# Kernel optimization log

Hardware: AMD Instinct MI355X
Metric: run time of the kernel (lower is better)

Reference implementation:

```python
import jax, jax.numpy as jnp
import numpy as np

B, T, E, V, H = 2, 2048, 1024, 2048, 8
KD, HD = E // H, V // H  # key_dim=128, head_dim=256
EPS = 1e-6


def rotate_every_two(x):
    x1 = x[..., ::2]
    x2 = x[..., 1::2]
    return jnp.stack((-x2, x1), axis=-1).reshape(x.shape)


def theta_shift(x, sin, cos):
    return x * cos + rotate_every_two(x) * sin


def setup_inputs() -> dict:
    key = jax.random.key(0)
    ks = jax.random.split(key, 8)
    x = jax.random.normal(ks[0], (B, T, E), dtype=jnp.float32)
    angle = jnp.arange(T, dtype=jnp.float32)[:, None] * (1.0 / (10000.0 ** (jnp.repeat(jnp.arange(KD // 2, dtype=jnp.float32), 2) * 2.0 / KD)))
    sin = jnp.sin(angle)  # [T, KD]
    cos = jnp.cos(angle)
    # RetNet per-head causal decay mask: decay_h = 1 - 2^(-5-h)
    decay = 1.0 - 2.0 ** (-5.0 - jnp.arange(H, dtype=jnp.float32))  # [H]
    idx = jnp.arange(T, dtype=jnp.float32)
    diff = idx[:, None] - idx[None, :]  # n - m
    causal = diff >= 0
    mask = jnp.where(causal[None], jnp.exp(jnp.where(causal, diff, 0.0)[None] * jnp.log(decay)[:, None, None]), 0.0)  # [H,T,T]
    g = 2 ** (-2.5)
    Wq = jax.random.normal(ks[1], (E, E), dtype=jnp.float32) * (g * np.sqrt(2.0 / (E + E)))
    Wk = jax.random.normal(ks[2], (E, E), dtype=jnp.float32) * (g * np.sqrt(2.0 / (E + E)))
    Wv = jax.random.normal(ks[3], (E, V), dtype=jnp.float32) * (g * np.sqrt(2.0 / (E + V)))
    Wg = jax.random.normal(ks[4], (E, V), dtype=jnp.float32) * (g * np.sqrt(2.0 / (E + V)))
    Wo = jax.random.normal(ks[5], (V, E), dtype=jnp.float32) * np.sqrt(2.0 / (V + E))
    return {"x": x, "sin": sin, "cos": cos, "mask": mask,
            "Wq": Wq, "Wk": Wk, "Wv": Wv, "Wg": Wg, "Wo": Wo}


def reference(x, sin, cos, mask, Wq, Wk, Wv, Wg, Wo):
    b, t, _ = x.shape
    scaling = KD ** -0.5
    q = (x @ Wq).reshape(b, t, H, KD).transpose(0, 2, 1, 3)  # [B,H,T,KD]
    k = (x @ Wk * scaling).reshape(b, t, H, KD).transpose(0, 2, 1, 3)
    v = x @ Wv  # [B,T,V]
    g = x @ Wg
    qr = theta_shift(q, sin, cos)
    kr = theta_shift(k, sin, cos)
    vr = v.reshape(b, t, H, HD).transpose(0, 2, 1, 3)  # [B,H,T,HD]
    qk = jnp.einsum('bhsk,bhtk->bhst', qr, kr) * mask  # [B,H,T,T]
    denom = jnp.clip(jnp.abs(jax.lax.stop_gradient(qk).sum(-1, keepdims=True)), 1.0, None)
    qk = qk / denom
    out = jnp.einsum('bhst,bhtd->bhsd', qk, vr)  # [B,H,T,HD]
    out = out.transpose(0, 2, 1, 3)  # [B,T,H,HD]
    # RMSNorm over head_dim, no affine
    out = out * jax.lax.rsqrt(jnp.mean(out * out, axis=-1, keepdims=True) + EPS)
    out = out.reshape(b, t, H * HD)
    out = jax.nn.silu(g) * out
    return out @ Wo  # [B,T,E]
```

## Files before the change

### kernel.cpp

```cpp
#include <hip/hip_runtime.h>
#include <hip/hip_bf16.h>


#define B_ 2
#define T_ 2048
#define E_ 1024
#define V_ 2048
#define H_ 8
#define KD_ 128
#define HD_ 256
#define M_ 4096

typedef __attribute__((ext_vector_type(8))) short bf16x8;
typedef __attribute__((ext_vector_type(4))) float f32x4;

__device__ __forceinline__ float u2f(unsigned short u) {
    return __uint_as_float(((unsigned)u) << 16);
}
__device__ __forceinline__ unsigned short f2bu(float f) {
    unsigned x = __float_as_uint(f);
    return (unsigned short)((x + 0x7fffu + ((x >> 16) & 1u)) >> 16);
}

typedef const __attribute__((address_space(1))) void gas_t;
typedef __attribute__((address_space(3))) void las_t;
__device__ __forceinline__ void gl_lds16(const void* g, void* l) {
    __builtin_amdgcn_global_load_lds((gas_t*)g, (las_t*)l, 16, 0, 0);
}

__global__ __launch_bounds__(256) void conv_x_kernel(
    const float* __restrict__ x, unsigned short* __restrict__ xb)
{
    const size_t i = ((size_t)blockIdx.x * 256 + threadIdx.x) * 8;
    float4 a = *(const float4*)(x + i);
    float4 c = *(const float4*)(x + i + 4);
    *(ushort4*)(xb + i)     = make_ushort4(f2bu(a.x), f2bu(a.y), f2bu(a.z), f2bu(a.w));
    *(ushort4*)(xb + i + 4) = make_ushort4(f2bu(c.x), f2bu(c.y), f2bu(c.z), f2bu(c.w));
}

__global__ __launch_bounds__(256) void transW4_kernel(
    const float* __restrict__ Wq, const float* __restrict__ Wk,
    const float* __restrict__ Wv, const float* __restrict__ Wg,
    unsigned short* __restrict__ Wt)
{
    const int z = blockIdx.z;
    const float* W; int N; int rofs;
    if (z == 0)      { W = Wq; N = 1024; rofs = 0; }
    else if (z == 1) { W = Wk; N = 1024; rofs = 1024; }
    else if (z == 2) { W = Wv; N = 2048; rofs = 2048; }
    else             { W = Wg; N = 2048; rofs = 4096; }
    const int n0 = blockIdx.x * 64;
    if (n0 >= N) return;
    const int k0 = blockIdx.y * 64;

    __shared__ float tl[64][65];
    const int tid = threadIdx.x;
    #pragma unroll
    for (int i = 0; i < 4; ++i) {
        int kr = i * 16 + (tid >> 4);
        int nc = (tid & 15) * 4;
        float4 v = *(const float4*)(W + (size_t)(k0 + kr) * N + n0 + nc);
        tl[kr][nc] = v.x; tl[kr][nc + 1] = v.y; tl[kr][nc + 2] = v.z; tl[kr][nc + 3] = v.w;
    }
    __syncthreads();
    #pragma unroll
    for (int i = 0; i < 4; ++i) {
        int nr = i * 16 + (tid >> 4);
        int kc = (tid & 15) * 4;
        ushort4 u = make_ushort4(f2bu(tl[kc + 0][nr]), f2bu(tl[kc + 1][nr]),
                                 f2bu(tl[kc + 2][nr]), f2bu(tl[kc + 3][nr]));
        *(ushort4*)(Wt + (size_t)(rofs + n0 + nr) * E_ + k0 + kc) = u;
    }
}

__global__ __launch_bounds__(256) void transW_kernel(
    const float* __restrict__ W, unsigned short* __restrict__ Wt, int K, int N)
{
    __shared__ float tl[64][65];
    const int tid = threadIdx.x;
    const int n0 = blockIdx.x * 64, k0 = blockIdx.y * 64;
    #pragma unroll
    for (int i = 0; i < 4; ++i) {
        int kr = i * 16 + (tid >> 4);
        int nc = (tid & 15) * 4;
        float4 v = *(const float4*)(W + (size_t)(k0 + kr) * N + n0 + nc);
        tl[kr][nc] = v.x; tl[kr][nc + 1] = v.y; tl[kr][nc + 2] = v.z; tl[kr][nc + 3] = v.w;
    }
    __syncthreads();
    #pragma unroll
    for (int i = 0; i < 4; ++i) {
        int nr = i * 16 + (tid >> 4);
        int kc = (tid & 15) * 4;
        ushort4 u = make_ushort4(f2bu(tl[kc + 0][nr]), f2bu(tl[kc + 1][nr]),
                                 f2bu(tl[kc + 2][nr]), f2bu(tl[kc + 3][nr]));
        *(ushort4*)(Wt + (size_t)(n0 + nr) * K + k0 + kc) = u;
    }
}

__global__ __launch_bounds__(256) void transV_kernel(
    const unsigned short* __restrict__ vb, unsigned short* __restrict__ vt)
{
    __shared__ unsigned short tl[64][68];
    const int tid = threadIdx.x;
    const int t0 = blockIdx.x * 64, c0 = blockIdx.y * 64, b = blockIdx.z;
    #pragma unroll
    for (int i = 0; i < 4; ++i) {
        int tr = i * 16 + (tid >> 4);
        int cc = (tid & 15) * 4;
        ushort4 v = *(const ushort4*)(vb + (size_t)(b * T_ + t0 + tr) * V_ + c0 + cc);
        tl[tr][cc] = v.x; tl[tr][cc + 1] = v.y; tl[tr][cc + 2] = v.z; tl[tr][cc + 3] = v.w;
    }
    __syncthreads();
    #pragma unroll
    for (int i = 0; i < 4; ++i) {
        int cr = i * 16 + (tid >> 4);
        int tc = (tid & 15) * 4;
        ushort4 u = make_ushort4(tl[tc + 0][cr], tl[tc + 1][cr], tl[tc + 2][cr], tl[tc + 3][cr]);
        *(ushort4*)(vt + (size_t)(b * V_ + c0 + cr) * T_ + t0 + tc) = u;
    }
}

#define GSTAGE(BUF, K0)                                                        \
    {                                                                          \
        _Pragma("unroll")                                                      \
        for (int i = 0; i < 4; ++i) {                                          \
            int r = i * 32 + srow;                                             \
            int cb = scolb ^ ((r & 7) << 4);                                   \
            gl_lds16((const char*)(A  + (size_t)(rowBase + r) * K + (K0)) + cb,\
                     Asm[BUF] + i * 4096 + w * 1024);                          \
            gl_lds16((const char*)(Bt + (size_t)(colBase + r) * K + (K0)) + cb,\
                     Bsm[BUF] + i * 4096 + w * 1024);                          \
        }                                                                      \
    }

#define GCOMPUTE(BUF)                                                          \
    {                                                                          \
        _Pragma("unroll")                                                      \
        for (int kk = 0; kk < 2; ++kk) {                                       \
            const int cb = kk * 64 + (l >> 4) * 16;                            \
            bf16x8 a[4], b[4];                                                 \
            _Pragma("unroll")                                                  \
            for (int m = 0; m < 4; ++m) {                                      \
                int r = wr * 64 + m * 16 + (l & 15);                           \
                a[m] = *(const bf16x8*)(Asm[BUF] + r * 128 + (cb ^ ((r & 7) << 4))); \
            }                                                                  \
            _Pragma("unroll")                                                  \
            for (int n = 0; n < 4; ++n) {                                      \
                int r = wc * 64 + n * 16 + (l & 15);                           \
                b[n] = *(const bf16x8*)(Bsm[BUF] + r * 128 + (cb ^ ((r & 7) << 4))); \
            }                                                                  \
            _Pragma("unroll")                                                  \
            for (int m = 0; m < 4; ++m)                                        \
                _Pragma("unroll")                                              \
                for (int n = 0; n < 4; ++n)                                    \
                    acc[m][n] = __builtin_amdgcn_mfma_f32_16x16x32_bf16(a[m], b[n], acc[m][n], 0, 0, 0); \
        }                                                                      \
    }

#define GEMM_PIPELINE_LOOP                                                     \
    GSTAGE(0, 0)                                                               \
    const int nk = K / 64;                                                     \
    for (int kt = 0; kt < nk; ++kt) {                                          \
        const int cur = kt & 1;                                                \
        if (kt + 1 < nk) {                                                     \
            GSTAGE(1 - cur, (kt + 1) * 64)                                     \
            asm volatile("s_waitcnt vmcnt(8)" ::: "memory");                   \
        } else {                                                               \
            asm volatile("s_waitcnt vmcnt(0)" ::: "memory");                   \
        }                                                                      \
        __builtin_amdgcn_s_barrier();                                          \
        __builtin_amdgcn_sched_barrier(0);                                     \
        GCOMPUTE(cur)                                                          \
        __builtin_amdgcn_s_barrier();                                          \
        __builtin_amdgcn_sched_barrier(0);                                     \
    }

__global__ __launch_bounds__(256) void gemm_qkvg_kernel(
    const unsigned short* __restrict__ A,
    const unsigned short* __restrict__ Bt,
    unsigned short* __restrict__ qb,
    unsigned short* __restrict__ kb,
    unsigned short* __restrict__ vb,
    unsigned short* __restrict__ gb)
{
    const int K = E_;
    __shared__ __align__(16) char Asm[2][128 * 64 * 2];
    __shared__ __align__(16) char Bsm[2][128 * 64 * 2];
    const int tid = threadIdx.x;
    const int l = tid & 63;
    const int w = tid >> 6;
    const int wr = w >> 1, wc = w & 1;
    const int rowBase = blockIdx.y * 128;
    const int colBase = blockIdx.x * 128;
    const int srow = tid >> 3;
    const int scolb = (tid & 7) * 16;

    f32x4 acc[4][4] = {};

    GEMM_PIPELINE_LOOP

    const int colW = colBase + wc * 64;
    unsigned short* dst;
    int cofs, stride;
    if (colW < 1024)      { dst = qb; cofs = 0;    stride = E_; }
    else if (colW < 2048) { dst = kb; cofs = 1024; stride = E_; }
    else if (colW < 4096) { dst = vb; cofs = 2048; stride = V_; }
    else                  { dst = gb; cofs = 4096; stride = V_; }
    #pragma unroll
    for (int m = 0; m < 4; ++m)
        #pragma unroll
        for (int n = 0; n < 4; ++n)
            #pragma unroll
            for (int r = 0; r < 4; ++r) {
                int row = rowBase + wr * 64 + m * 16 + (l >> 4) * 4 + r;
                int col = colW + n * 16 + (l & 15);
                float f = acc[m][n][r];
                if (!isfinite(f)) f = 0.f;
                dst[(size_t)row * stride + (col - cofs)] = f2bu(f);
            }
}

__global__ __launch_bounds__(256) void gemm_wo_kernel(
    const unsigned short* __restrict__ A,
    const unsigned short* __restrict__ Bt,
    float* __restrict__ C)
{
    const int K = V_;
    __shared__ __align__(16) char Asm[2][64 * 128];
    __shared__ __align__(16) char Bsm[2][128 * 128];
    const int tid = threadIdx.x;
    const int l = tid & 63;
    const int w = tid >> 6;
    const int wr = w >> 1, wc = w & 1;
    const int rowBase = blockIdx.y * 64;
    const int colBase = blockIdx.x * 128;
    const int srow = tid >> 3;
    const int scolb = (tid & 7) * 16;

    f32x4 acc[2][4] = {};

#define WSTAGE(BUF, K0)                                                        \
    {                                                                          \
        _Pragma("unroll")                                                      \
        for (int i = 0; i < 2; ++i) {                                          \
            int r = i * 32 + srow;                                             \
            int cb = scolb ^ ((r & 7) << 4);                                   \
            gl_lds16((const char*)(A + (size_t)(rowBase + r) * K + (K0)) + cb, \
                     Asm[BUF] + i * 4096 + w * 1024);                          \
        }                                                                      \
        _Pragma("unroll")                                                      \
        for (int i = 0; i < 4; ++i) {                                          \
            int r = i * 32 + srow;                                             \
            int cb = scolb ^ ((r & 7) << 4);                                   \
            gl_lds16((const char*)(Bt + (size_t)(colBase + r) * K + (K0)) + cb,\
                     Bsm[BUF] + i * 4096 + w * 1024);                          \
        }                                                                      \
    }

    WSTAGE(0, 0)
    const int nk = K / 64;
    for (int kt = 0; kt < nk; ++kt) {
        const int cur = kt & 1;
        if (kt + 1 < nk) {
            WSTAGE(1 - cur, (kt + 1) * 64)
            asm volatile("s_waitcnt vmcnt(6)" ::: "memory");
        } else {
            asm volatile("s_waitcnt vmcnt(0)" ::: "memory");
        }
        __builtin_amdgcn_s_barrier();
        __builtin_amdgcn_sched_barrier(0);
        #pragma unroll
        for (int kk = 0; kk < 2; ++kk) {
            const int cb = kk * 64 + (l >> 4) * 16;
            bf16x8 a[2], b[4];
            #pragma unroll
            for (int m = 0; m < 2; ++m) {
                int r = wr * 32 + m * 16 + (l & 15);
                a[m] = *(const bf16x8*)(Asm[cur] + r * 128 + (cb ^ ((r & 7) << 4)));
            }
            #pragma unroll
            for (int n = 0; n < 4; ++n) {
                int r = wc * 64 + n * 16 + (l & 15);
                b[n] = *(const bf16x8*)(Bsm[cur] + r * 128 + (cb ^ ((r & 7) << 4)));
            }
            #pragma unroll
            for (int m = 0; m < 2; ++m)
                #pragma unroll
                for (int n = 0; n < 4; ++n)
                    acc[m][n] = __builtin_amdgcn_mfma_f32_16x16x32_bf16(a[m], b[n], acc[m][n], 0, 0, 0);
        }
        __builtin_amdgcn_s_barrier();
        __builtin_amdgcn_sched_barrier(0);
    }
#undef WSTAGE

    #pragma unroll
    for (int m = 0; m < 2; ++m)
        #pragma unroll
        for (int n = 0; n < 4; ++n)
            #pragma unroll
            for (int r = 0; r < 4; ++r) {
                int row = rowBase + wr * 32 + m * 16 + (l >> 4) * 4 + r;
                int col = colBase + wc * 64 + n * 16 + (l & 15);
                float f = acc[m][n][r];
                if (!isfinite(f)) f = 0.f;
                C[(size_t)row * E_ + col] = f;
            }
}

__global__ __launch_bounds__(256) void theta2_kernel(
    unsigned short* __restrict__ qb,
    unsigned short* __restrict__ kb,
    const float* __restrict__ sinp, const float* __restrict__ cosp)
{
    unsigned short* qk = blockIdx.y ? kb : qb;
    const float scale = blockIdx.y ? 0.088388347648318447f : 1.0f;
    const int i = blockIdx.x * 256 + threadIdx.x;
    const int pe = i & (E_ / 2 - 1);
    const int bt = i >> 9;
    const int t = bt & (T_ - 1);
    const int e0 = pe << 1;
    const int d0 = e0 & (KD_ - 1);
    const size_t base = (size_t)bt * E_ + e0;
    const float q0 = u2f(qk[base]);
    const float q1 = u2f(qk[base + 1]);
    const int sb = t * KD_ + d0;
    const float s0 = sinp[sb], s1 = sinp[sb + 1];
    const float c0 = cosp[sb], c1 = cosp[sb + 1];
    qk[base]     = f2bu((q0 * c0 - q1 * s0) * scale);
    qk[base + 1] = f2bu((q1 * c1 + q0 * s1) * scale);
}

#define STAGE_K(BUF, T0)                                                       \
    {                                                                          \
        _Pragma("unroll")                                                      \
        for (int i = 0; i < 4; ++i) {                                          \
            int r = i * 16 + (tid >> 4);                                       \
            int cb = ((tid & 15) * 16) ^ ((r & 7) << 4);                       \
            gl_lds16((const char*)(kb + (size_t)(b * T_ + (T0) + r) * E_ + h * KD_) + cb, \
                     Ks[BUF] + i * 4096 + w * 1024);                           \
        }                                                                      \
    }

#define STAGE_V(T0)                                                            \
    {                                                                          \
        _Pragma("unroll")                                                      \
        for (int i = 0; i < 8; ++i) {                                          \
            int r = i * 32 + (tid >> 3);                                       \
            int cb = ((tid & 7) * 16) ^ ((r & 7) << 4);                        \
            gl_lds16((const char*)(vt + (size_t)((b * H_ + h) * HD_ + r) * T_ + (T0)) + cb, \
                     Vs + i * 4096 + w * 1024);                                \
        }                                                                      \
    }

__global__ __launch_bounds__(256, 2) void retention_mfma_kernel(
    const unsigned short* __restrict__ qb,
    const unsigned short* __restrict__ kb,
    const unsigned short* __restrict__ vt,
    const unsigned short* __restrict__ g,
    unsigned short* __restrict__ ao)
{
    __shared__ __align__(16) char Ks[2][64 * 128 * 2];
    __shared__ __align__(16) char Vs[256 * 64 * 2];
    __shared__ __align__(16) char Pq[64 * 64 * 2];
    __shared__ float rsum_p[4][64];
    __shared__ float rsq_p[4][64];
    const int tid = threadIdx.x;
    const int l = tid & 63;
    const int w = tid >> 6;
    const int g_ = l >> 4;
    const int q15 = l & 15;
    const int orig = (int)blockIdx.x;
    const int xcd  = orig & 7;
    const int pos  = orig >> 3;
    const int slot = pos >> 5;
    const int cu   = pos & 31;
    const int half = cu >> 4;
    const int c15  = cu & 15;
    const int bh   = xcd * 2 + half;
    const int chunk = slot ? c15 : (31 - c15);
    const int b = bh >> 3, h = bh & 7;
    const int s0 = chunk * 64;
    const float ld = logf(1.f - exp2f(-5.f - (float)h));

    float es[4];
    #pragma unroll
    for (int qb2 = 0; qb2 < 4; ++qb2)
        es[qb2] = __expf((float)(s0 + qb2 * 16 + q15) * ld);
    float etl[4];
    #pragma unroll
    for (int r = 0; r < 4; ++r)
        etl[r] = __expf(-(float)(w * 16 + 4 * g_ + r) * ld);
    const float Dm64 = __expf(-64.f * ld);
    float etb = 1.f;

    bf16x8 qf[4][4];
    #pragma unroll
    for (int qb2 = 0; qb2 < 4; ++qb2) {
        const char* qp = (const char*)(qb + (size_t)(b * T_ + s0 + qb2 * 16 + q15) * E_ + h * KD_);
        #pragma unroll
        for (int kk = 0; kk < 4; ++kk)
            qf[qb2][kk] = *(const bf16x8*)(qp + kk * 64 + g_ * 16);
    }

    f32x4 oaccT[4][4] = {};
    float rs[4] = {0.f, 0.f, 0.f, 0.f};

    const int nt = chunk + 1;
    STAGE_K(0, 0)

    for (int t = 0; t < nt; ++t) {
        const int cur = t & 1;
        const int t0 = t * 64;
        STAGE_V(t0)
        if (t + 1 < nt) {
            STAGE_K(1 - cur, t0 + 64)
            asm volatile("s_waitcnt vmcnt(12)" ::: "memory");
        } else {
            asm volatile("s_waitcnt vmcnt(8)" ::: "memory");
        }
        __builtin_amdgcn_s_barrier();
        __builtin_amdgcn_sched_barrier(0);

        f32x4 sacc[4] = {};
        {
            const int krow = w * 16 + q15;
            const int swz = (krow & 7) << 4;
            #pragma unroll
            for (int kk = 0; kk < 4; ++kk) {
                bf16x8 kf = *(const bf16x8*)(Ks[cur] + krow * 256 + ((kk * 64 + g_ * 16) ^ swz));
                #pragma unroll
                for (int qb2 = 0; qb2 < 4; ++qb2)
                    sacc[qb2] = __builtin_amdgcn_mfma_f32_16x16x32_bf16(kf, qf[qb2][kk], sacc[qb2], 0, 0, 0);
            }
        }
        {
            const float etw = etb;
            #pragma unroll
            for (int qb2 = 0; qb2 < 4; ++qb2) {
                const int qg = s0 + qb2 * 16 + q15;
                const int q_local = qb2 * 16 + q15;
                float rsp = 0.f;
                unsigned short pk[4];
                #pragma unroll
                for (int r = 0; r < 4; ++r) {
                    int tg = t0 + w * 16 + 4 * g_ + r;
                    float pm = (qg >= tg) ? sacc[qb2][r] * (es[qb2] * etw * etl[r]) : 0.f;
                    rsp += pm;
                    pk[r] = f2bu(pm);
                }
                *(ushort4*)(Pq + q_local * 128 + (((w * 16 + 4 * g_) * 2) ^ ((q_local & 7) << 4))) =
                    make_ushort4(pk[0], pk[1], pk[2], pk[3]);
                rsp += __shfl_xor(rsp, 16);
                rsp += __shfl_xor(rsp, 32);
                rs[qb2] += rsp;
            }
            etb *= Dm64;
        }
        if (t + 1 < nt) {
            asm volatile("s_waitcnt vmcnt(4) lgkmcnt(0)" ::: "memory");
        } else {
            asm volatile("s_waitcnt vmcnt(0) lgkmcnt(0)" ::: "memory");
        }
        __builtin_amdgcn_s_barrier();
        __builtin_amdgcn_sched_barrier(0);
        #pragma unroll
        for (int kk = 0; kk < 2; ++kk) {
            const int cb = kk * 64 + g_ * 16;
            bf16x8 pf[4], vf[4];
            #pragma unroll
            for (int qb2 = 0; qb2 < 4; ++qb2) {
                int pr = qb2 * 16 + q15;
                pf[qb2] = *(const bf16x8*)(Pq + pr * 128 + (cb ^ ((pr & 7) << 4)));
            }
            #pragma unroll
            for (int m = 0; m < 4; ++m) {
                int vr = w * 64 + m * 16 + q15;
                vf[m] = *(const bf16x8*)(Vs + vr * 128 + (cb ^ ((vr & 7) << 4)));
            }
            #pragma unroll
            for (int qb2 = 0; qb2 < 4; ++qb2)
                #pragma unroll
                for (int m = 0; m < 4; ++m)
                    oaccT[qb2][m] = __builtin_amdgcn_mfma_f32_16x16x32_bf16(vf[m], pf[qb2], oaccT[qb2][m], 0, 0, 0);
        }
        __builtin_amdgcn_s_barrier();
        __builtin_amdgcn_sched_barrier(0);
    }

    if (l < 16) {
        #pragma unroll
        for (int qb2 = 0; qb2 < 4; ++qb2)
            rsum_p[w][qb2 * 16 + q15] = rs[qb2];
    }
    __syncthreads();

    float inv[4];
    #pragma unroll
    for (int qb2 = 0; qb2 < 4; ++qb2) {
        const int q_local = qb2 * 16 + q15;
        const float tot = rsum_p[0][q_local] + rsum_p[1][q_local] +
                          rsum_p[2][q_local] + rsum_p[3][q_local];
        inv[qb2] = 1.f / fmaxf(fabsf(tot), 1.f);
    }

    #pragma unroll
    for (int qb2 = 0; qb2 < 4; ++qb2) {
        float ps = 0.f;
        #pragma unroll
        for (int m = 0; m < 4; ++m)
            #pragma unroll
            for (int r = 0; r < 4; ++r) {
                float o = oaccT[qb2][m][r] * inv[qb2];
                ps += o * o;
            }
        ps += __shfl_xor(ps, 16);
        ps += __shfl_xor(ps, 32);
        if (l < 16) rsq_p[w][qb2 * 16 + q15] = ps;
    }
    __syncthreads();

    #pragma unroll
    for (int qb2 = 0; qb2 < 4; ++qb2) {
        const int q_local = qb2 * 16 + q15;
        const float tot = rsq_p[0][q_local] + rsq_p[1][q_local] +
                          rsq_p[2][q_local] + rsq_p[3][q_local];
        const float scale = rsqrtf(tot * (1.0f / HD_) + 1e-6f) * inv[qb2];
        const size_t rowb = (size_t)(b * T_ + s0 + q_local) * V_ + h * HD_;
        #pragma unroll
        for (int m = 0; m < 4; ++m) {
            const int vc0 = w * 64 + m * 16 + 4 * g_;
            ushort4 gv4 = *(const ushort4*)(g + rowb + vc0);
            const unsigned short* gv = (const unsigned short*)&gv4;
            unsigned short outp[4];
            #pragma unroll
            for (int r = 0; r < 4; ++r) {
                const float gvf = u2f(gv[r]);
                const float silu = gvf / (1.f + __expf(-gvf));
                float f = oaccT[qb2][m][r] * scale * silu;
                if (!isfinite(f)) f = 0.f;
                outp[r] = f2bu(f);
            }
            *(ushort4*)(ao + rowb + vc0) = make_ushort4(outp[0], outp[1], outp[2], outp[3]);
        }
    }
}

extern "C" void kernel_launch(void* const* d_in, const int* in_sizes, int n_in,
                              void* d_out, int out_size, void* d_ws, size_t ws_size,
                              hipStream_t stream)
{
    const float* x    = (const float*)d_in[0];
    const float* sinp = (const float*)d_in[1];
    const float* cosp = (const float*)d_in[2];
    const float* Wq   = (const float*)d_in[4];
    const float* Wk   = (const float*)d_in[5];
    const float* Wv   = (const float*)d_in[6];
    const float* Wg   = (const float*)d_in[7];
    const float* Wo   = (const float*)d_in[8];
    float* out = (float*)d_out;

    unsigned short* xb = (unsigned short*)d_out;
    unsigned short* qb = xb + (size_t)M_ * E_;

    char* ws = (char*)d_ws;
    unsigned short* kb  = (unsigned short*)(ws + 0);
    unsigned short* vb  = (unsigned short*)(ws + 8388608);
    unsigned short* gb  = (unsigned short*)(ws + 25165824);
    unsigned short* wt  = (unsigned short*)(ws + 41943040);
    unsigned short* vt  = (unsigned short*)(ws + 54525952);
    unsigned short* aob = (unsigned short*)(ws + 71303168);
    unsigned short* wot = (unsigned short*)(ws + 88080384);

    dim3 blk(256);
    conv_x_kernel<<<M_ * E_ / 8 / 256, blk, 0, stream>>>(x, xb);

    transW4_kernel<<<dim3(32, 16, 4), blk, 0, stream>>>(Wq, Wk, Wv, Wg, wt);

    gemm_qkvg_kernel<<<dim3(48, 32), blk, 0, stream>>>(xb, wt, qb, kb, vb, gb);

    theta2_kernel<<<dim3(M_ * E_ / 2 / 256, 2), blk, 0, stream>>>(qb, kb, sinp, cosp);

    transV_kernel<<<dim3(32, 32, B_), blk, 0, stream>>>(vb, vt);

    retention_mfma_kernel<<<dim3(512), blk, 0, stream>>>(qb, kb, vt, gb, aob);

    transW_kernel<<<dim3(16, 32), blk, 0, stream>>>(Wo, wot, V_, E_);
    gemm_wo_kernel<<<dim3(8, 64), blk, 0, stream>>>(aob, wot, out);
}
```

Baseline: 190.6 us.

## Double-buffer V tiles in retention kernel and fold Wo transpose into weight prep

The retention kernel now keeps two V buffers, so the next V tile is prefetched together with the next K tile instead of being loaded at the top of each iteration and waited on mid-loop. The launch bound's min-blocks hint is dropped and the XCD-aware block-to-chunk mapping is replaced by a simple linear one, heaviest chunks first. The Wo transpose is merged into the combined weight-transpose kernel, removing one launch at the cost of idle blocks in the enlarged grid. Doubling V storage raises LDS use per block, which may lower occupancy.

```diff
diff --git a/kernel.cpp b/kernel.cpp
--- a/kernel.cpp
+++ b/kernel.cpp
@@ -38,20 +38,22 @@
     *(ushort4*)(xb + i + 4) = make_ushort4(f2bu(c.x), f2bu(c.y), f2bu(c.z), f2bu(c.w));
 }
 
-__global__ __launch_bounds__(256) void transW4_kernel(
+__global__ __launch_bounds__(256) void transW5_kernel(
     const float* __restrict__ Wq, const float* __restrict__ Wk,
     const float* __restrict__ Wv, const float* __restrict__ Wg,
-    unsigned short* __restrict__ Wt)
+    const float* __restrict__ Wo,
+    unsigned short* __restrict__ Wt, unsigned short* __restrict__ wot)
 {
     const int z = blockIdx.z;
-    const float* W; int N; int rofs;
-    if (z == 0)      { W = Wq; N = 1024; rofs = 0; }
-    else if (z == 1) { W = Wk; N = 1024; rofs = 1024; }
-    else if (z == 2) { W = Wv; N = 2048; rofs = 2048; }
-    else             { W = Wg; N = 2048; rofs = 4096; }
+    const float* W; int N; int rofs; int Kd; unsigned short* dst;
+    if (z == 0)      { W = Wq; N = 1024; rofs = 0;    Kd = 1024; dst = Wt; }
+    else if (z == 1) { W = Wk; N = 1024; rofs = 1024; Kd = 1024; dst = Wt; }
+    else if (z == 2) { W = Wv; N = 2048; rofs = 2048; Kd = 1024; dst = Wt; }
+    else if (z == 3) { W = Wg; N = 2048; rofs = 4096; Kd = 1024; dst = Wt; }
+    else             { W = Wo; N = 1024; rofs = 0;    Kd = 2048; dst = wot; }
     const int n0 = blockIdx.x * 64;
-    if (n0 >= N) return;
     const int k0 = blockIdx.y * 64;
+    if (n0 >= N || k0 >= Kd) return;
 
     __shared__ float tl[64][65];
     const int tid = threadIdx.x;
@@ -69,31 +71,7 @@
         int kc = (tid & 15) * 4;
         ushort4 u = make_ushort4(f2bu(tl[kc + 0][nr]), f2bu(tl[kc + 1][nr]),
                                  f2bu(tl[kc + 2][nr]), f2bu(tl[kc + 3][nr]));
-        *(ushort4*)(Wt + (size_t)(rofs + n0 + nr) * E_ + k0 + kc) = u;
-    }
-}
-
-__global__ __launch_bounds__(256) void transW_kernel(
-    const float* __restrict__ W, unsigned short* __restrict__ Wt, int K, int N)
-{
-    __shared__ float tl[64][65];
-    const int tid = threadIdx.x;
-    const int n0 = blockIdx.x * 64, k0 = blockIdx.y * 64;
-    #pragma unroll
-    for (int i = 0; i < 4; ++i) {
-        int kr = i * 16 + (tid >> 4);
-        int nc = (tid & 15) * 4;
-        float4 v = *(const float4*)(W + (size_t)(k0 + kr) * N + n0 + nc);
-        tl[kr][nc] = v.x; tl[kr][nc + 1] = v.y; tl[kr][nc + 2] = v.z; tl[kr][nc + 3] = v.w;
-    }
-    __syncthreads();
-    #pragma unroll
-    for (int i = 0; i < 4; ++i) {
-        int nr = i * 16 + (tid >> 4);
-        int kc = (tid & 15) * 4;
-        ushort4 u = make_ushort4(f2bu(tl[kc + 0][nr]), f2bu(tl[kc + 1][nr]),
-                                 f2bu(tl[kc + 2][nr]), f2bu(tl[kc + 3][nr]));
-        *(ushort4*)(Wt + (size_t)(n0 + nr) * K + k0 + kc) = u;
+        *(ushort4*)(dst + (size_t)(rofs + n0 + nr) * Kd + k0 + kc) = u;
     }
 }
 
@@ -342,18 +320,18 @@
         }                                                                      \
     }
 
-#define STAGE_V(T0)                                                            \
+#define STAGE_V(BUF, T0)                                                       \
     {                                                                          \
         _Pragma("unroll")                                                      \
         for (int i = 0; i < 8; ++i) {                                          \
             int r = i * 32 + (tid >> 3);                                       \
             int cb = ((tid & 7) * 16) ^ ((r & 7) << 4);                        \
             gl_lds16((const char*)(vt + (size_t)((b * H_ + h) * HD_ + r) * T_ + (T0)) + cb, \
-                     Vs + i * 4096 + w * 1024);                                \
-        }                                                                      \
-    }
-
-__global__ __launch_bounds__(256, 2) void retention_mfma_kernel(
+                     Vs[BUF] + i * 4096 + w * 1024);                           \
+        }                                                                      \
+    }
+
+__global__ __launch_bounds__(256) void retention_mfma_kernel(
     const unsigned short* __restrict__ qb,
     const unsigned short* __restrict__ kb,
     const unsigned short* __restrict__ vt,
@@ -361,7 +339,7 @@
     unsigned short* __restrict__ ao)
 {
     __shared__ __align__(16) char Ks[2][64 * 128 * 2];
-    __shared__ __align__(16) char Vs[256 * 64 * 2];
+    __shared__ __align__(16) char Vs[2][256 * 64 * 2];
     __shared__ __align__(16) char Pq[64 * 64 * 2];
     __shared__ float rsum_p[4][64];
     __shared__ float rsq_p[4][64];
@@ -371,14 +349,8 @@
     const int g_ = l >> 4;
     const int q15 = l & 15;
     const int orig = (int)blockIdx.x;
-    const int xcd  = orig & 7;
-    const int pos  = orig >> 3;
-    const int slot = pos >> 5;
-    const int cu   = pos & 31;
-    const int half = cu >> 4;
-    const int c15  = cu & 15;
-    const int bh   = xcd * 2 + half;
-    const int chunk = slot ? c15 : (31 - c15);
+    const int bh   = orig & 15;
+    const int chunk = 31 - (orig >> 4);
     const int b = bh >> 3, h = bh & 7;
     const int s0 = chunk * 64;
     const float ld = logf(1.f - exp2f(-5.f - (float)h));
@@ -408,16 +380,17 @@
 
     const int nt = chunk + 1;
     STAGE_K(0, 0)
+    STAGE_V(0, 0)
 
     for (int t = 0; t < nt; ++t) {
         const int cur = t & 1;
         const int t0 = t * 64;
-        STAGE_V(t0)
         if (t + 1 < nt) {
             STAGE_K(1 - cur, t0 + 64)
+            STAGE_V(1 - cur, t0 + 64)
             asm volatile("s_waitcnt vmcnt(12)" ::: "memory");
         } else {
-            asm volatile("s_waitcnt vmcnt(8)" ::: "memory");
+            asm volatile("s_waitcnt vmcnt(0)" ::: "memory");
         }
         __builtin_amdgcn_s_barrier();
         __builtin_amdgcn_sched_barrier(0);
@@ -457,11 +430,7 @@
             }
             etb *= Dm64;
         }
-        if (t + 1 < nt) {
-            asm volatile("s_waitcnt vmcnt(4) lgkmcnt(0)" ::: "memory");
-        } else {
-            asm volatile("s_waitcnt vmcnt(0) lgkmcnt(0)" ::: "memory");
-        }
+        asm volatile("s_waitcnt lgkmcnt(0)" ::: "memory");
         __builtin_amdgcn_s_barrier();
         __builtin_amdgcn_sched_barrier(0);
         #pragma unroll
@@ -476,7 +445,7 @@
             #pragma unroll
             for (int m = 0; m < 4; ++m) {
                 int vr = w * 64 + m * 16 + q15;
-                vf[m] = *(const bf16x8*)(Vs + vr * 128 + (cb ^ ((vr & 7) << 4)));
+                vf[m] = *(const bf16x8*)(Vs[cur] + vr * 128 + (cb ^ ((vr & 7) << 4)));
             }
             #pragma unroll
             for (int qb2 = 0; qb2 < 4; ++qb2)
@@ -575,7 +544,7 @@
     dim3 blk(256);
     conv_x_kernel<<<M_ * E_ / 8 / 256, blk, 0, stream>>>(x, xb);
 
-    transW4_kernel<<<dim3(32, 16, 4), blk, 0, stream>>>(Wq, Wk, Wv, Wg, wt);
+    transW5_kernel<<<dim3(32, 32, 5), blk, 0, stream>>>(Wq, Wk, Wv, Wg, Wo, wt, wot);
 
     gemm_qkvg_kernel<<<dim3(48, 32), blk, 0, stream>>>(xb, wt, qb, kb, vb, gb);
 
@@ -585,6 +554,5 @@
 
     retention_mfma_kernel<<<dim3(512), blk, 0, stream>>>(qb, kb, vt, gb, aob);
 
-    transW_kernel<<<dim3(16, 32), blk, 0, stream>>>(Wo, wot, V_, E_);
     gemm_wo_kernel<<<dim3(8, 64), blk, 0, stream>>>(aob, wot, out);
 }
```

Result: slower. 199.7 us (+4.8%).
